# Kernel tuning notes

Hardware: AMD Instinct MI355X
Metric: run time of the kernel (lower is better)

## Reference

```python
import jax, jax.numpy as jnp
import numpy as np

B, N, CIN = 8, 1024, 2048
HID, HC, LV = 1024, 64, 512
NH_SSD, HD, DS = 16, 128, 64
DCONV = 4

def layernorm(x, w, b, eps=1e-5):
    m = x.mean(-1, keepdims=True)
    v = ((x - m) ** 2).mean(-1, keepdims=True)
    return (x - m) * jax.lax.rsqrt(v + eps) * w + b

def rmsnorm(x, w, eps=1e-5):
    return x * jax.lax.rsqrt((x * x).mean(-1, keepdims=True) + eps) * w

def segsum(a):
    # a: (..., T) -> (..., T, T); [i,j] = sum_{j<k<=i} a[k]; -inf above diagonal
    T = a.shape[-1]
    cs = jnp.cumsum(a, -1)
    seg = cs[..., :, None] - cs[..., None, :]
    i = jnp.arange(T)
    return jnp.where(i[:, None] >= i[None, :], seg, -jnp.inf)

def mha(x, Wq, Wk, Wv, Wo, Wo_b, nh=4):
    b, s, h = x.shape
    hd = h // nh
    q = (x @ Wq.T).reshape(b, s, nh, hd).transpose(0, 2, 1, 3)
    k = (x @ Wk.T).reshape(b, s, nh, hd).transpose(0, 2, 1, 3)
    v = (x @ Wv.T).reshape(b, s, nh, hd).transpose(0, 2, 1, 3)
    att = jax.nn.softmax(jnp.einsum('bhqd,bhkd->bhqk', q, k) / jnp.sqrt(jnp.float32(hd)), axis=-1)
    o = jnp.einsum('bhqk,bhkd->bhqd', att, v).transpose(0, 2, 1, 3).reshape(b, s, h)
    return o @ Wo.T + Wo_b

def ssd_minimal(X, A, Bv, Cv, Lc):
    # faithful ssd_minimal_discrete; Bv/Cv have ngroups=1 broadcast to heads (torch einsum broadcasts size-1 labels)
    b, T, h, p = X.shape
    c = T // Lc
    n = Bv.shape[-1]
    X = X.reshape(b, c, Lc, h, p)
    A = A.reshape(b, c, Lc, h).transpose(0, 3, 1, 2)  # b h c l
    Bv = jnp.broadcast_to(Bv.reshape(b, c, Lc, 1, n), (b, c, Lc, h, n))
    Cv = jnp.broadcast_to(Cv.reshape(b, c, Lc, 1, n), (b, c, Lc, h, n))
    cs = jnp.cumsum(A, -1)
    Lmat = jnp.exp(segsum(A))  # b h c l s
    Yd = jnp.einsum('bclhn,bcshn,bhcls,bcshp->bclhp', Cv, Bv, Lmat, X)
    dstates = jnp.exp(cs[..., -1:] - cs)
    st = jnp.einsum('bclhn,bhcl,bclhp->bchpn', Bv, dstates, X)
    st = jnp.concatenate([jnp.zeros_like(st[:, :1]), st], axis=1)
    dchunk = jnp.exp(segsum(jnp.pad(cs[..., -1], ((0, 0), (0, 0), (1, 0)))))
    st = jnp.einsum('bhzc,bchpn->bzhpn', dchunk, st)[:, :-1]
    Yo = jnp.einsum('bclhn,bchpn,bhcl->bclhp', Cv, st, jnp.exp(cs))
    return (Yd + Yo).reshape(b, T, h, p)

def ssd_block(xc, xproj_W, dt_bias, A_log, D):
    b, l, d = xc.shape
    dtBC = xc @ xproj_W.T
    dt = jax.nn.softplus(dtBC[..., :NH_SSD] + dt_bias)
    Bm = dtBC[..., NH_SSD:NH_SSD + DS]
    Cm = dtBC[..., NH_SSD + DS:]
    A = -jnp.exp(A_log)
    X = xc.reshape(b, l, NH_SSD, HD) * dt[..., None]
    Y = ssd_minimal(X, A * dt, Bm, Cm, l)  # single chunk: Lc = seqlen (as in SSD.forward)
    return Y.reshape(b, l, d) + xc * jnp.repeat(D, HD)

@jax.custom_vjp
def round3(y):
    return jnp.round(y)

def _r3_fwd(y):
    return jnp.round(y), y

def _r3_bwd(y, g):
    return (g * (y != 0).astype(g.dtype),)

round3.defvjp(_r3_fwd, _r3_bwd)

def _forward(x, ln0_w, ln0_b, in_W, rms_w, exp_W, conv_W, xproj_W, dt_bias, A_log, D,
             outp_W, outp_b, n1_w, n1_b, aWq, aWk, aWv, aWo, aWo_b,
             h_W, h_b, h_lnw, h_lnb, mask_token, e2d_W, dn_w, dn_b,
             bWq, bWk, bWv, bWo, bWo_b, dout_W, dout_b, mask):
    b = x.shape[0]
    # visible tokens: mask==False; stable argsort keeps original order (== x[~mask].reshape(B,-1,C))
    vis = jnp.argsort(mask.astype(jnp.int32), axis=1)[:, :LV]
    xv = jnp.take_along_axis(x, vis[:, :, None], axis=1)
    xv = layernorm(xv, ln0_w, ln0_b)
    h = xv @ in_W.T
    t = h
    h = rmsnorm(h, rms_w)
    xz = h @ exp_W.T
    xs, z = xz[..., :2 * HID], xz[..., 2 * HID:]
    xc = jax.lax.conv_general_dilated(
        xs.transpose(0, 2, 1), conv_W, (1,), [(DCONV - 1, DCONV - 1)],
        dimension_numbers=('NCH', 'OIH', 'NCH'), feature_group_count=HID)[:, :, :LV].transpose(0, 2, 1)
    y = ssd_block(xc, xproj_W, dt_bias, A_log, D)
    y = y * jax.nn.silu(z)
    y = y @ outp_W.T + outp_b + t
    y = y + mha(layernorm(y, n1_w, n1_b), aWq, aWk, aWv, aWo, aWo_b)
    # hash layer: LN -> hard sigmoid -> straight-through round -> {-1,+1}
    hc = layernorm(y @ h_W.T + h_b, h_lnw, h_lnb)
    hc = 2.0 * round3(jnp.clip((hc + 1.0) / 2.0, 0.0, 1.0)) - 1.0
    # decoder: visible codes + mask tokens
    Lm = N - LV
    dx = jnp.concatenate([hc, jnp.broadcast_to(mask_token, (b, Lm, HC))], axis=1)
    dx = dx @ e2d_W.T
    dx = dx + mha(layernorm(dx, dn_w, dn_b), bWq, bWk, bWv, bWo, bWo_b)
    out = dx @ dout_W.T + dout_b
    return out[:, -Lm:]

def setup_inputs():
    key = jax.random.key(0)
    ks = jax.random.split(key, 20)
    r = lambda i, shape, s=0.02: jax.random.normal(ks[i], shape, dtype=jnp.float32) * s
    x = jax.random.normal(ks[0], (B, N, CIN), dtype=jnp.float32)
    mask = jnp.concatenate([jnp.zeros((B, LV), bool), jnp.ones((B, N - LV), bool)], axis=1)
    A = jax.random.uniform(ks[1], (NH_SSD,), minval=1.0, maxval=16.0)
    return dict(
        x=x,
        ln0_w=jnp.ones(CIN), ln0_b=jnp.zeros(CIN),
        in_W=r(2, (HID, CIN)),
        rms_w=jnp.ones(HID),
        exp_W=r(3, (4 * HID, HID)),
        conv_W=r(4, (2 * HID, 2, DCONV), 0.1),
        xproj_W=r(5, (NH_SSD + 2 * DS, 2 * HID)),
        dt_bias=jnp.zeros(NH_SSD), A_log=jnp.log(A), D=jnp.ones(NH_SSD),
        outp_W=r(6, (HID, 2 * HID)), outp_b=jnp.zeros(HID),
        n1_w=jnp.ones(HID), n1_b=jnp.zeros(HID),
        aWq=r(7, (HID, HID)), aWk=r(8, (HID, HID)), aWv=r(9, (HID, HID)),
        aWo=r(10, (HID, HID)), aWo_b=jnp.zeros(HID),
        h_W=r(11, (HC, HID)), h_b=jnp.zeros(HC),
        h_lnw=jnp.ones(HC), h_lnb=jnp.zeros(HC),
        mask_token=jnp.zeros((1, 1, HC)),
        e2d_W=r(12, (HID, HC)),
        dn_w=jnp.ones(HID), dn_b=jnp.zeros(HID),
        bWq=r(13, (HID, HID)), bWk=r(14, (HID, HID)), bWv=r(15, (HID, HID)),
        bWo=r(16, (HID, HID)), bWo_b=jnp.zeros(HID),
        dout_W=r(17, (CIN, HID)), dout_b=jnp.zeros(CIN),
        mask=mask)

def reference(x, ln0_w, ln0_b, in_W, rms_w, exp_W, conv_W, xproj_W, dt_bias, A_log, D,
              outp_W, outp_b, n1_w, n1_b, aWq, aWk, aWv, aWo, aWo_b,
              h_W, h_b, h_lnw, h_lnb, mask_token, e2d_W, dn_w, dn_b,
              bWq, bWk, bWv, bWo, bWo_b, dout_W, dout_b, mask):
    return _forward(x, ln0_w, ln0_b, in_W, rms_w, exp_W, conv_W, xproj_W, dt_bias, A_log, D,
                    outp_W, outp_b, n1_w, n1_b, aWq, aWk, aWv, aWo, aWo_b,
                    h_W, h_b, h_lnw, h_lnb, mask_token, e2d_W, dn_w, dn_b,
                    bWq, bWk, bWv, bWo, bWo_b, dout_W, dout_b, mask)
```

## Files before the change

kernel.cpp:

```cpp
#include <hip/hip_runtime.h>


typedef short bf16x8 __attribute__((ext_vector_type(8)));
typedef float f32x4 __attribute__((ext_vector_type(4)));

__device__ __forceinline__ unsigned short bf16_rne(float f) {
    unsigned u = __float_as_uint(f);
    unsigned r = u + 0x7FFFu + ((u >> 16) & 1u);
    return (unsigned short)(r >> 16);
}
__device__ __forceinline__ float bf16_tof(unsigned short h) {
    return __uint_as_float(((unsigned)h) << 16);
}
__device__ __forceinline__ void store_pair(unsigned short* dst, long long row,
                                           int width, int c, float v) {
    unsigned short hi = bf16_rne(v);
    unsigned short lo = bf16_rne(v - bf16_tof(hi));
    long long base = row * (2LL * width);
    dst[base + c] = hi;
    dst[base + width + c] = lo;
}
__device__ __forceinline__ void async_ld16(const unsigned short* g, unsigned short* l) {
    __builtin_amdgcn_global_load_lds(
        (const __attribute__((address_space(1))) unsigned int*)g,
        (__attribute__((address_space(3))) unsigned int*)l, 16, 0, 0);
}

__device__ __forceinline__ void xcd_remap(int& bx, int& by) {
    const int Gx = gridDim.x;
    const int nwg = Gx * gridDim.y;
    if ((nwg & 7) != 0) return;
    int lin = bx + Gx * by;
    int logical = (lin & 7) * (nwg >> 3) + (lin >> 3);
    bx = logical % Gx;
    by = logical / Gx;
}

__device__ __forceinline__ float block_sum256(float v) {
    #pragma unroll
    for (int o = 32; o > 0; o >>= 1) v += __shfl_xor(v, o, 64);
    __shared__ float sm[4];
    int w = threadIdx.x >> 6;
    __syncthreads();
    if ((threadIdx.x & 63) == 0) sm[w] = v;
    __syncthreads();
    return sm[0] + sm[1] + sm[2] + sm[3];
}
__device__ __forceinline__ float block_max256(float v) {
    #pragma unroll
    for (int o = 32; o > 0; o >>= 1) v = fmaxf(v, __shfl_xor(v, o, 64));
    __shared__ float smx[4];
    int w = threadIdx.x >> 6;
    __syncthreads();
    if ((threadIdx.x & 63) == 0) smx[w] = v;
    __syncthreads();
    return fmaxf(fmaxf(smx[0], smx[1]), fmaxf(smx[2], smx[3]));
}

template<int NPASS, int OUT, bool DIRECT>
__global__ __launch_bounds__(256, 2) void gemm_bf16_k(
    int M, int N, int K,
    const unsigned short* __restrict__ A2, int lda2, int aLo, long long sAb, long long sAh,
    const unsigned short* __restrict__ B2, int ldb2, int bLo, long long sBb, long long sBh,
    void* __restrict__ Cv, int ldc, int cLo, long long sCb, long long sCh,
    const float* __restrict__ bias, const float* __restrict__ res, int ldr,
    float alpha, int nh)
{
    constexpr int ST   = DIRECT ? 32 : 40;
    constexpr int NARR = (NPASS == 3) ? 4 : 2;
    constexpr int NB   = DIRECT ? 2 : 1;
    constexpr int O_AH = 0;
    constexpr int O_BH = 128 * ST;
    constexpr int O_AL = 2 * 128 * ST;
    constexpr int O_BL = 3 * 128 * ST;
    constexpr int BUFSZ = 128 * ST * NARR;
    __shared__ unsigned short SM[NB * BUFSZ];

    const int z  = blockIdx.z;
    const int bb = z / nh, hh = z - bb * nh;
    A2 += bb * sAb + hh * sAh;
    B2 += bb * sBb + hh * sBh;

    int bx = blockIdx.x, by = blockIdx.y;
    xcd_remap(bx, by);
    const int t    = threadIdx.x;
    const int m0   = by * 128;
    const int n0   = bx * 128;
    const int lane = t & 63, wave = t >> 6;
    const int wm   = (wave >> 1) * 64, wn = (wave & 1) * 64;
    const int lr   = lane & 15, quad = lane >> 4;

    f32x4 acc[4][4];
    #pragma unroll
    for (int i = 0; i < 4; ++i)
        #pragma unroll
        for (int j = 0; j < 4; ++j) acc[i][j] = (f32x4){0.f, 0.f, 0.f, 0.f};

    if constexpr (DIRECT) {
        const int drow  = lane >> 2;
        const int dcswz = (((lane & 3) ^ ((lane >> 2) & 3) ^ ((lane >> 4) & 3)) << 3);
        const int rsw   = ((quad ^ ((lr & 3) ^ (lr >> 2))) << 3);

        auto stage = [&](int k0, int buf) {
            unsigned short* bp = &SM[buf * BUFSZ];
            #pragma unroll
            for (int j = 0; j < 2; ++j) {
                int rr = wave * 32 + j * 16;
                int gr = rr + drow;
                const unsigned short* gA = A2 + (long long)(m0 + gr) * lda2 + k0 + dcswz;
                async_ld16(gA, &bp[O_AH + rr * 32]);
                if (NPASS == 3) async_ld16(gA + aLo, &bp[O_AL + rr * 32]);
                const unsigned short* gB = B2 + (long long)(n0 + gr) * ldb2 + k0 + dcswz;
                async_ld16(gB, &bp[O_BH + rr * 32]);
                if (NPASS == 3) async_ld16(gB + bLo, &bp[O_BL + rr * 32]);
            }
        };

        const int nt = K >> 5;
        stage(0, 0);
        int cur = 0;
        for (int it = 0; it < nt; ++it) {
            asm volatile("s_waitcnt vmcnt(0)" ::: "memory");
            __builtin_amdgcn_s_barrier();
            if (it + 1 < nt) stage((it + 1) << 5, cur ^ 1);

            const unsigned short* bp = &SM[cur * BUFSZ];
            bf16x8 ah[4], bh[4], al[4], bl[4];
            #pragma unroll
            for (int i = 0; i < 4; ++i) {
                int ra = O_AH + (wm + i * 16 + lr) * 32 + rsw;
                int rb = O_BH + (wn + i * 16 + lr) * 32 + rsw;
                ah[i] = *(const bf16x8*)&bp[ra];
                bh[i] = *(const bf16x8*)&bp[rb];
                if (NPASS == 3) {
                    al[i] = *(const bf16x8*)&bp[ra + (O_AL - O_AH)];
                    bl[i] = *(const bf16x8*)&bp[rb + (O_BL - O_BH)];
                }
            }
            #pragma unroll
            for (int mi = 0; mi < 4; ++mi)
                #pragma unroll
                for (int ni = 0; ni < 4; ++ni) {
                    acc[mi][ni] = __builtin_amdgcn_mfma_f32_16x16x32_bf16(
                        ah[mi], bh[ni], acc[mi][ni], 0, 0, 0);
                    if (NPASS == 3) {
                        acc[mi][ni] = __builtin_amdgcn_mfma_f32_16x16x32_bf16(
                            al[mi], bh[ni], acc[mi][ni], 0, 0, 0);
                        acc[mi][ni] = __builtin_amdgcn_mfma_f32_16x16x32_bf16(
                            ah[mi], bl[ni], acc[mi][ni], 0, 0, 0);
                    }
                }
            cur ^= 1;
        }
    } else {
        const int srow = t >> 2;
        const int scol = (t & 3) * 8;

        for (int k0 = 0; k0 < K; k0 += 32) {
            __syncthreads();
            #pragma unroll
            for (int half = 0; half < 2; ++half) {
                int r = srow + half * 64;
                const unsigned short* pA = A2 + (long long)(m0 + r) * lda2 + k0 + scol;
                *(uint4*)&SM[O_AH + r * ST + scol] = *(const uint4*)pA;
                if (NPASS == 3)
                    *(uint4*)&SM[O_AL + r * ST + scol] = *(const uint4*)(pA + aLo);
                int rb = n0 + r;
                uint4 vh = {0u, 0u, 0u, 0u}, vl = {0u, 0u, 0u, 0u};
                if (rb < N) {
                    const unsigned short* pB = B2 + (long long)rb * ldb2 + k0 + scol;
                    vh = *(const uint4*)pB;
                    if (NPASS == 3) vl = *(const uint4*)(pB + bLo);
                }
                *(uint4*)&SM[O_BH + r * ST + scol] = vh;
                if (NPASS == 3) *(uint4*)&SM[O_BL + r * ST + scol] = vl;
            }
            __syncthreads();

            bf16x8 ah[4], bh[4], al[4], bl[4];
            #pragma unroll
            for (int i = 0; i < 4; ++i) {
                int ra = (wm + i * 16 + lr) * ST + quad * 8;
                int rb = (wn + i * 16 + lr) * ST + quad * 8;
                ah[i] = *(const bf16x8*)&SM[O_AH + ra];
                bh[i] = *(const bf16x8*)&SM[O_BH + rb];
                if (NPASS == 3) {
                    al[i] = *(const bf16x8*)&SM[O_AL + ra];
                    bl[i] = *(const bf16x8*)&SM[O_BL + rb];
                }
            }
            #pragma unroll
            for (int mi = 0; mi < 4; ++mi)
                #pragma unroll
                for (int ni = 0; ni < 4; ++ni) {
                    acc[mi][ni] = __builtin_amdgcn_mfma_f32_16x16x32_bf16(
                        ah[mi], bh[ni], acc[mi][ni], 0, 0, 0);
                    if (NPASS == 3) {
                        acc[mi][ni] = __builtin_amdgcn_mfma_f32_16x16x32_bf16(
                            al[mi], bh[ni], acc[mi][ni], 0, 0, 0);
                        acc[mi][ni] = __builtin_amdgcn_mfma_f32_16x16x32_bf16(
                            ah[mi], bl[ni], acc[mi][ni], 0, 0, 0);
                    }
                }
        }
    }

    if (OUT == 0) {
        float* C = (float*)Cv + bb * sCb + hh * sCh;
        #pragma unroll
        for (int mi = 0; mi < 4; ++mi)
            #pragma unroll
            for (int ni = 0; ni < 4; ++ni) {
                int col = n0 + wn + ni * 16 + lr;
                if (col >= N) continue;
                float bv = bias ? bias[col] : 0.f;
                #pragma unroll
                for (int r = 0; r < 4; ++r) {
                    int row = m0 + wm + mi * 16 + quad * 4 + r;
                    float v = alpha * acc[mi][ni][r] + bv;
                    if (res) v += res[(long long)row * ldr + col];
                    C[(long long)row * ldc + col] = v;
                }
            }
    } else if (OUT == 1) {
        unsigned short* C = (unsigned short*)Cv + bb * sCb + hh * sCh;
        #pragma unroll
        for (int mi = 0; mi < 4; ++mi)
            #pragma unroll
            for (int ni = 0; ni < 4; ++ni) {
                int col = n0 + wn + ni * 16 + lr;
                if (col >= N) continue;
                float bv = bias ? bias[col] : 0.f;
                #pragma unroll
                for (int r = 0; r < 4; ++r) {
                    int row = m0 + wm + mi * 16 + quad * 4 + r;
                    float v = alpha * acc[mi][ni][r] + bv;
                    if (res) v += res[(long long)row * ldr + col];
                    unsigned short hi = bf16_rne(v);
                    unsigned short lo = bf16_rne(v - bf16_tof(hi));
                    long long p = (long long)row * ldc + col;
                    C[p] = hi;
                    C[p + cLo] = lo;
                }
            }
    } else {
        unsigned short* C = (unsigned short*)Cv;
        #pragma unroll
        for (int mi = 0; mi < 4; ++mi)
            #pragma unroll
            for (int ni = 0; ni < 4; ++ni) {
                int col = n0 + wn + ni * 16 + lr;
                if (col >= N) continue;
                int row0 = m0 + wm + mi * 16 + quad * 4;
                int b = row0 >> 9, seq0 = row0 & 511;
                ushort4 h4, l4;
// ... 174 lines not shown
            if (rb < N) {
                const unsigned short* pB = B2 + (long long)rb * ldb2 + k0 + scol;
                vh = *(const uint4*)pB;
                if (NPASS == 3) vl = *(const uint4*)(pB + bLo);
            }
            *(uint4*)&Bh[r * ST + scol] = vh;
            if (NPASS == 3) *(uint4*)&Bl[r * ST + scol] = vl;
        }
        __syncthreads();

        bf16x8 ah[4], bh[4], al[4], bl[4];
        #pragma unroll
        for (int i = 0; i < 4; ++i) {
            int ra = (wm + i * 16 + lr) * ST + quad * 8;
            int rb = (wn + i * 16 + lr) * ST + quad * 8;
            ah[i] = *(const bf16x8*)&Ah[ra];
            bh[i] = *(const bf16x8*)&Bh[rb];
            if (NPASS == 3) {
                al[i] = *(const bf16x8*)&Al[ra];
                bl[i] = *(const bf16x8*)&Bl[rb];
            }
        }
        #pragma unroll
        for (int mi = 0; mi < 4; ++mi)
            #pragma unroll
            for (int ni = 0; ni < 4; ++ni) {
                acc[mi][ni] = __builtin_amdgcn_mfma_f32_16x16x32_bf16(
                    ah[mi], bh[ni], acc[mi][ni], 0, 0, 0);
                if (NPASS == 3) {
                    acc[mi][ni] = __builtin_amdgcn_mfma_f32_16x16x32_bf16(
                        al[mi], bh[ni], acc[mi][ni], 0, 0, 0);
                    acc[mi][ni] = __builtin_amdgcn_mfma_f32_16x16x32_bf16(
                        ah[mi], bl[ni], acc[mi][ni], 0, 0, 0);
                }
            }
    }

    float* Cc = C + (long long)blockIdx.z * sCk;
    #pragma unroll
    for (int mi = 0; mi < 4; ++mi)
        #pragma unroll
        for (int ni = 0; ni < 4; ++ni) {
            int col = n0 + wn + ni * 16 + lr;
            if (col >= N) continue;
            #pragma unroll
            for (int r = 0; r < 4; ++r) {
                int row = m0 + wm + mi * 16 + quad * 4 + r;
                Cc[(long long)row * N + col] = acc[mi][ni][r];
            }
        }
}


__global__ __launch_bounds__(256) void skred_rms_k(
    const float* __restrict__ P, long long sCk,
    float* __restrict__ T, unsigned short* __restrict__ HR2,
    const float* __restrict__ w)
{
    long long r = blockIdx.x;
    const int t = threadIdx.x;
    long long base = r * 1024 + t * 4;
    float4 a = *(const float4*)&P[base];
    float4 bq = *(const float4*)&P[sCk + base];
    float v[4] = {a.x + bq.x, a.y + bq.y, a.z + bq.z, a.w + bq.w};
    *(float4*)&T[base] = *(float4*)v;
    float s = v[0]*v[0] + v[1]*v[1] + v[2]*v[2] + v[3]*v[3];
    s = block_sum256(s);
    float rs = 1.f / sqrtf(s * (1.f / 1024.f) + 1e-5f);
    #pragma unroll
    for (int e = 0; e < 4; ++e) {
        int c = t * 4 + e;
        store_pair(HR2, r, 1024, c, v[e] * rs * w[c]);
    }
}

__global__ __launch_bounds__(256) void skred_ln_k(
    const float* __restrict__ P, long long sCk,
    const float* __restrict__ bias, const float* __restrict__ res,
    float* __restrict__ Y1, unsigned short* __restrict__ LNY2,
    const float* __restrict__ w, const float* __restrict__ b)
{
    long long r = blockIdx.x;
    const int t = threadIdx.x;
    long long base = r * 1024 + t * 4;
    float4 a  = *(const float4*)&P[base];
    float4 bq = *(const float4*)&P[sCk + base];
    float4 rv = *(const float4*)&res[base];
    float4 bi = *(const float4*)&bias[t * 4];
    float v[4] = {a.x + bq.x + rv.x + bi.x, a.y + bq.y + rv.y + bi.y,
                  a.z + bq.z + rv.z + bi.z, a.w + bq.w + rv.w + bi.w};
    *(float4*)&Y1[base] = *(float4*)v;
    float s = v[0] + v[1] + v[2] + v[3];
    s = block_sum256(s);
    float m = s * (1.f / 1024.f);
    float vs = 0.f;
    #pragma unroll
    for (int e = 0; e < 4; ++e) { float d = v[e] - m; vs += d * d; }
    vs = block_sum256(vs);
    float rs = 1.f / sqrtf(vs * (1.f / 1024.f) + 1e-5f);
    #pragma unroll
    for (int e = 0; e < 4; ++e) {
        int c = t * 4 + e;
        store_pair(LNY2, r, 1024, c, (v[e] - m) * rs * w[c] + b[c]);
    }
}

__global__ __launch_bounds__(256) void skred_dt_k(
    const float* __restrict__ P, long long sCk,
    const float* __restrict__ dt_bias,
    float* __restrict__ dtBC, float* __restrict__ DT, long long n)
{
    long long idx = (long long)blockIdx.x * 256 + threadIdx.x;
    if (idx >= n) return;
// ... 176 lines not shown
        if (nt > 1) asm volatile("s_waitcnt vmcnt(4)" ::: "memory");
        else        asm volatile("s_waitcnt vmcnt(0)" ::: "memory");
        asm volatile("s_waitcnt lgkmcnt(0)" ::: "memory");
        __builtin_amdgcn_s_barrier();

        for (int it = 0; it < nt; ++it) {
            const int xb = it % 3;
            const int wb = it & 1;
            if (it + 1 < nt) gen_load((it + 1) << 5);
            if (it + 2 < nt) stageX((it + 2) << 5, (it + 2) % 3);

            bf16x8 ah = *(const bf16x8*)&Wh[wb][fbase];
            bf16x8 al = *(const bf16x8*)&Wl[wb][fbase];
            const unsigned short* xhp = &Xh[xb][0];
            const unsigned short* xlp = &Xl[xb][0];
            #pragma unroll
            for (int ni = 0; ni < 8; ++ni) {
                int base = (ni * 16 + lr) * 32 + xsw;
                bf16x8 bh = *(const bf16x8*)&xhp[base];
                bf16x8 bl = *(const bf16x8*)&xlp[base];
                acc[ni] = __builtin_amdgcn_mfma_f32_16x16x32_bf16(
                    ah, bh, acc[ni], 0, 0, 0);
                acc[ni] = __builtin_amdgcn_mfma_f32_16x16x32_bf16(
                    al, bh, acc[ni], 0, 0, 0);
                acc[ni] = __builtin_amdgcn_mfma_f32_16x16x32_bf16(
                    ah, bl, acc[ni], 0, 0, 0);
            }
            if (it + 1 < nt) gen_finish((it + 1) << 5, wb ^ 1);
            if (it + 2 < nt) asm volatile("s_waitcnt vmcnt(4)" ::: "memory");
            else             asm volatile("s_waitcnt vmcnt(0)" ::: "memory");
            asm volatile("s_waitcnt lgkmcnt(0)" ::: "memory");
            __builtin_amdgcn_s_barrier();
        }

        const int row0 = m0 + wave * 16 + quad * 4;
        #pragma unroll
        for (int ni = 0; ni < 8; ++ni) {
            int chan = h * 128 + ni * 16 + lr;
            #pragma unroll
            for (int r = 0; r < 4; ++r) {
                long long row = (long long)(b * 512 + row0 + r);
                float zz = Z[row * 2048 + chan];
                float y = acc[ni][r] * (zz / (1.f + expf(-zz)));
                store_pair(YS2, row, 2048, chan, y);
            }
        }
    }
}

__global__ __launch_bounds__(256) void gemm_f32_k(
    int M, int N, int K,
    const float* __restrict__ A, int lda, long long sAb,
    const float* __restrict__ B, int ldb, long long sBb,
    float* __restrict__ C, int ldc, long long sCb)
{
    __shared__ float As[32][132];
    __shared__ float Bs[32][132];
    const int z = blockIdx.z;
    A += z * sAb; B += z * sBb; C += z * sCb;
    const int n0 = blockIdx.x * 128;
    const int m0 = blockIdx.y * 128;
    const int t  = threadIdx.x;
    const int tx = t & 15, ty = t >> 4;

    float acc[4][16];
    #pragma unroll
    for (int a = 0; a < 4; ++a)
        #pragma unroll
        for (int q = 0; q < 16; ++q) acc[a][q] = 0.f;

    const int ka = (t & 7) << 2;
    const int ra = t >> 3;

    for (int k0 = 0; k0 < K; k0 += 32) {
        __syncthreads();
        #pragma unroll
        for (int i = 0; i < 4; ++i) {
            int row = m0 + ra + i * 32;
            float4 v = *(const float4*)(A + (long long)row * lda + (k0 + ka));
            As[ka + 0][ra + i * 32] = v.x;
            As[ka + 1][ra + i * 32] = v.y;
            As[ka + 2][ra + i * 32] = v.z;
            As[ka + 3][ra + i * 32] = v.w;
            int rowb = n0 + ra + i * 32;
            float4 w = *(const float4*)(B + (long long)rowb * ldb + (k0 + ka));
            Bs[ka + 0][ra + i * 32] = w.x;
            Bs[ka + 1][ra + i * 32] = w.y;
            Bs[ka + 2][ra + i * 32] = w.z;
            Bs[ka + 3][ra + i * 32] = w.w;
        }
        __syncthreads();
        #pragma unroll
        for (int kk = 0; kk < 32; ++kk) {
            float a[8], bm[8];
            *(float4*)&a[0]  = *(const float4*)&As[kk][ty * 4];
            *(float4*)&a[4]  = *(const float4*)&As[kk][64 + ty * 4];
            *(float4*)&bm[0] = *(const float4*)&Bs[kk][tx * 4];
            *(float4*)&bm[4] = *(const float4*)&Bs[kk][64 + tx * 4];
            #pragma unroll
            for (int ri = 0; ri < 2; ++ri)
                #pragma unroll
                for (int ci = 0; ci < 2; ++ci)
                    #pragma unroll
                    for (int i = 0; i < 4; ++i)
                        #pragma unroll
                        for (int j = 0; j < 4; ++j)
                            acc[ri * 2 + ci][i * 4 + j] =
                                fmaf(a[ri * 4 + i], bm[ci * 4 + j], acc[ri * 2 + ci][i * 4 + j]);
        }
    }
    #pragma unroll
    for (int ri = 0; ri < 2; ++ri)
        #pragma unroll
        for (int ci = 0; ci < 2; ++ci) {
            int colb = n0 + ci * 64 + tx * 4;
            #pragma unroll
            for (int i = 0; i < 4; ++i) {
                int row = m0 + ri * 64 + ty * 4 + i;
                *(float4*)(C + (long long)row * ldc + colb) =
                    *(float4*)&acc[ri * 2 + ci][i * 4];
            }
        }
}

__global__ __launch_bounds__(256) void pairify_k(
    const float* __restrict__ src, unsigned short* __restrict__ dst,
    int k_log2, long long n)
{
    long long idx = (long long)blockIdx.x * 256 + threadIdx.x;
    if (idx >= n) return;
    long long r = idx >> k_log2;
    int c = (int)(idx & ((1 << k_log2) - 1));
    store_pair(dst, r, 1 << k_log2, c, src[idx]);
}

struct PairSegs {
    const float* src[7];
    unsigned short* dst[7];
    long long n[7];
    int klog2[7];
};
__global__ __launch_bounds__(256) void pairify_multi_k(PairSegs segs)
{
    int sg = blockIdx.y;
    long long idx = (long long)blockIdx.x * 256 + threadIdx.x;
    if (idx >= segs.n[sg]) return;
    int kl = segs.klog2[sg];
    long long r = idx >> kl;
    int c = (int)(idx & ((1LL << kl) - 1));
    store_pair(segs.dst[sg], r, 1 << kl, c, segs.src[sg][idx]);
}

template<int NE>
__global__ __launch_bounds__(256) void layernorm_pair_v_k(
    const float* __restrict__ in, unsigned short* __restrict__ out2,
    const float* __restrict__ w, const float* __restrict__ b,
    int rows_per_b, long long in_bstride)
{
    const int width = NE * 256;
    long long r = blockIdx.x;
    const float* x = in + (r / rows_per_b) * in_bstride
                   + (r % rows_per_b) * (long long)width;
    const int t = threadIdx.x;
    float v[NE];
    float s = 0.f;
    #pragma unroll
    for (int j = 0; j < NE / 4; ++j) {
        float4 f = *(const float4*)(x + j * 1024 + t * 4);
        v[j * 4 + 0] = f.x; v[j * 4 + 1] = f.y;
        v[j * 4 + 2] = f.z; v[j * 4 + 3] = f.w;
        s += f.x + f.y + f.z + f.w;
    }
    s = block_sum256(s);
    float m = s / (float)width;
    float vs = 0.f;
    #pragma unroll
    for (int e = 0; e < NE; ++e) { float d = v[e] - m; vs += d * d; }
    vs = block_sum256(vs);
    float rs = 1.f / sqrtf(vs / (float)width + 1e-5f);
    #pragma unroll
    for (int j = 0; j < NE / 4; ++j)
        #pragma unroll
        for (int e = 0; e < 4; ++e) {
            int c = j * 1024 + t * 4 + e;
            store_pair(out2, r, width, c, (v[j * 4 + e] - m) * rs * w[c] + b[c]);
        }
}

__global__ __launch_bounds__(256) void softmax_pair_k(float* __restrict__ S,
                                                      unsigned short* __restrict__ P2)
{
    long long r = blockIdx.x;
    float* x = S + r * 512;
    unsigned short* p = P2 + r * 1024;
    int t = threadIdx.x;
    float v0 = x[t], v1 = x[t + 256];
    float mx = block_max256(fmaxf(v0, v1));
    v0 = expf(v0 - mx); v1 = expf(v1 - mx);
    float sum = block_sum256(v0 + v1);
    float inv = 1.f / sum;
    v0 *= inv; v1 *= inv;
    __syncthreads();
    unsigned short h0 = bf16_rne(v0);
    p[t] = h0;       p[512 + t] = bf16_rne(v0 - bf16_tof(h0));
    unsigned short h1 = bf16_rne(v1);
    p[t + 256] = h1; p[512 + t + 256] = bf16_rne(v1 - bf16_tof(h1));
}

__global__ __launch_bounds__(256) void conv_k(
    const float* __restrict__ XS, const float* __restrict__ W,
    unsigned short* __restrict__ XC2, unsigned short* __restrict__ XCT2)
{
    __shared__ float tile[64][65];
    const int o0  = blockIdx.x * 64;
    const int tt0 = blockIdx.y * 64;
    const int b   = blockIdx.z;
    const int t   = threadIdx.x;

    const int o  = o0 + (t & 63);
    const int g2 = (o >> 1) << 1;
    const float* Wo = W + o * 8;
    float w0 = Wo[0], w1 = Wo[1], w2 = Wo[2], w3 = Wo[3];
    float w4 = Wo[4], w5 = Wo[5], w6 = Wo[6], w7 = Wo[7];
    #pragma unroll
    for (int i = 0; i < 16; ++i) {
        int sl = (t >> 6) + 4 * i;
        int tt = tt0 + sl;
        const float* xb = XS + ((long long)(b * 512 + tt)) * 2048 + g2;
        float acc = w3 * xb[0] + w7 * xb[1];
        if (tt >= 1) acc += w2 * xb[-2048] + w6 * xb[-2047];
        if (tt >= 2) acc += w1 * xb[-4096] + w5 * xb[-4095];
        if (tt >= 3) acc += w0 * xb[-6144] + w4 * xb[-6143];
        tile[sl][t & 63] = acc;
    }
    __syncthreads();
    #pragma unroll
    for (int i = 0; i < 16; ++i) {
        int idx = t + 256 * i;
        int sl = idx >> 6, ol = idx & 63;
        float v = tile[sl][ol];
        unsigned short hi = bf16_rne(v);
        unsigned short lo = bf16_rne(v - bf16_tof(hi));
        long long row = (long long)(b * 512 + tt0 + sl);
        XC2[row * 4096 + o0 + ol] = hi;
        XC2[row * 4096 + 2048 + o0 + ol] = lo;
    }
    #pragma unroll
    for (int i = 0; i < 16; ++i) {
        int idx = t + 256 * i;
        int cl = idx >> 6, s = idx & 63;
        float v = tile[s][cl];
        unsigned short hi = bf16_rne(v);
        unsigned short lo = bf16_rne(v - bf16_tof(hi));
        long long tb = (long long)b * 2097152 + (long long)(o0 + cl) * 1024 + tt0 + s;
        XCT2[tb] = hi;
        XCT2[tb + 512] = lo;
    }
}

__global__ __launch_bounds__(64) void cuma_k(
    const float* __restrict__ DT, const float* __restrict__ A_log, float* __restrict__ CUMA)
{
    int h = blockIdx.x, b = blockIdx.y;
    int ln = threadIdx.x;
    float Ah = -expf(A_log[h]);
    float v[8];
    float run = 0.f;
    #pragma unroll
    for (int i = 0; i < 8; ++i) {
        run += Ah * DT[((b * 512) + (ln * 8 + i)) * 16 + h];
        v[i] = run;
    }
    float tot = run;
    float sc = tot;
    #pragma unroll
    for (int o = 1; o <= 32; o <<= 1) {
        float u = __shfl_up(sc, o, 64);
        if (ln >= o) sc += u;
    }
    float excl = sc - tot;
    #pragma unroll
    for (int i = 0; i < 8; ++i)
        CUMA[(b * 16 + h) * 512 + ln * 8 + i] = excl + v[i];
}

__global__ __launch_bounds__(256) void dxm_ln_k(
    const float* __restrict__ mtok, const float* __restrict__ e2d,
    const float* __restrict__ w, const float* __restrict__ b,
    float* __restrict__ dxm, float* __restrict__ lnm)
{
    __shared__ float dx[1024];
    const int t = threadIdx.x;
    float mv[64];
    #pragma unroll
    for (int j = 0; j < 64; ++j) mv[j] = mtok[j];
    float loc[4];
    #pragma unroll
    for (int q = 0; q < 4; ++q) {
        int c = q * 256 + t;
        const float* er = e2d + (long long)c * 64;
        float acc = 0.f;
        #pragma unroll
        for (int j = 0; j < 64; ++j) acc = fmaf(mv[j], er[j], acc);
        loc[q] = acc;
        dx[c] = acc;
        dxm[c] = acc;
    }
    float s = loc[0] + loc[1] + loc[2] + loc[3];
    s = block_sum256(s);
    float m = s * (1.f / 1024.f);
    float vs = 0.f;
    #pragma unroll
    for (int q = 0; q < 4; ++q) { float d = loc[q] - m; vs += d * d; }
    vs = block_sum256(vs);
    float rs = 1.f / sqrtf(vs * (1.f / 1024.f) + 1e-5f);
    #pragma unroll
    for (int q = 0; q < 4; ++q) {
        int c = q * 256 + t;
        lnm[c] = (loc[q] - m) * rs * w[c] + b[c];
    }
}

__global__ __launch_bounds__(256) void projm_k(
    const float* __restrict__ lnm,
    const float* __restrict__ bWq, const float* __restrict__ bWk, const float* __restrict__ bWv,
    float* __restrict__ qm, float* __restrict__ km, float* __restrict__ vm)
{
    int idx = blockIdx.x * 256 + threadIdx.x;
    int sel = idx >> 10, c = idx & 1023;
    const float* W = (sel == 0) ? bWq : (sel == 1) ? bWk : bWv;
    float* O = (sel == 0) ? qm : (sel == 1) ? km : vm;
    const float* wr = W + (long long)c * 1024;
    float acc = 0.f;
    for (int j = 0; j < 1024; j += 4) {
        float4 a = *(const float4*)(lnm + j);
        float4 w4 = *(const float4*)(wr + j);
        acc = fmaf(a.x, w4.x, fmaf(a.y, w4.y, fmaf(a.z, w4.z, fmaf(a.w, w4.w, acc))));
    }
    O[c] = acc;
}

__global__ __launch_bounds__(256) void dec_attn_k(
    const float* __restrict__ KVm,
    const float* __restrict__ qm, const float* __restrict__ km,
    const float* __restrict__ vm, float* __restrict__ OBm)
{
    int h = blockIdx.x, b = blockIdx.y;
    int t = threadIdx.x;
    __shared__ __align__(16) float qs[256];
    __shared__ __align__(16) float ps[512];
    qs[t] = qm[h * 256 + t];
    __syncthreads();
    float s[2];
    #pragma unroll
    for (int i = 0; i < 2; ++i) {
        int r = t + i * 256;
        const float* kr = KVm + ((long long)(b * 512 + r)) * 2048 + h * 256;
        float acc = 0.f;
        for (int c = 0; c < 256; c += 4) {
            float4 k4 = *(const float4*)(kr + c);
            float4 q4 = *(const float4*)(qs + c);
            acc = fmaf(k4.x, q4.x, fmaf(k4.y, q4.y, fmaf(k4.z, q4.z, fmaf(k4.w, q4.w, acc))));
        }
        s[i] = acc * (1.f / 16.f);
    }
    float accm = 0.f;
    for (int c = 0; c < 256; c += 4) {
        float4 k4 = *(const float4*)(km + h * 256 + c);
        float4 q4 = *(const float4*)(qs + c);
        accm = fmaf(k4.x, q4.x, fmaf(k4.y, q4.y, fmaf(k4.z, q4.z, fmaf(k4.w, q4.w, accm))));
    }
    float smv = accm * (1.f / 16.f);
// ... 114 lines not shown
    unsigned short* XCT2    = (unsigned short*)S1;
    float*          POUTP   = S1;
    float*          SA      = S1;
    unsigned short* P2      = (unsigned short*)S1;
    float*          KVm     = S1;
    unsigned short* in_W2   = (unsigned short*)S2;
    float*          XS      = S2;
    unsigned short* YS2     = (unsigned short*)S2;
    float*          PX      = S2;
    unsigned short* QKA2    = (unsigned short*)S2;
    unsigned short* XC2     = (unsigned short*)S3;
    float*          PIN     = S3;
    unsigned short* outp_W2 = (unsigned short*)S3;
    float*          PATT    = S3;
    float*          PH      = S3;
    float*          DXV     = S3;
    unsigned short* LNDXV2  = (unsigned short*)(S3 + 4194304);
    float*          Z       = S4;
    unsigned short* aWq2    = (unsigned short*)S4;
    unsigned short* aWk2    = (unsigned short*)S4 + 2097152;
    unsigned short* aWv2    = (unsigned short*)S4 + 4194304;
    unsigned short* aWo2    = (unsigned short*)S4 + 6291456;
    unsigned short* bWk2    = (unsigned short*)S4 + 8388608;
    unsigned short* bWv2    = (unsigned short*)S4 + 10485760;
    float*          T       = S5;
    unsigned short* Y22     = (unsigned short*)S5;
    unsigned short* HR2     = (unsigned short*)S6;
    float*          Y1      = S6;
    unsigned short* LNY2    = (unsigned short*)S7;
    unsigned short* OA2     = (unsigned short*)S7;
    unsigned short* VT2     = (unsigned short*)S9;

    float* dtBC = SP;
    float* DT   = SP + 589824;
    float* CUMA = SP + 655360;
    float* G    = SP + 720896;
    unsigned short* xprojW2 = (unsigned short*)(SP + 2818048);
    unsigned short* hW2     = (unsigned short*)(SP + 3112960);
    unsigned short* e2dW2   = (unsigned short*)(SP + 3178496);
    unsigned short* HCQ2 = (unsigned short*)(SP + 983040);
    float* dxm  = SP + 1245184;
    float* lnm  = SP + 1246208;
    float* qm   = SP + 1247232;
    float* km   = SP + 1248256;
    float* vm   = SP + 1249280;
    float* OBm  = SP + 1250304;
    float* ydm  = SP + 1258496;
    float* outm = SP + 1266688;

    const long long LL0 = 0;
    const long long P4M = 4194304;
    #define G3D(OUTM, GX, GY, GZ, ...) \
        gemm_bf16_k<3, OUTM, true><<<dim3(GX, GY, GZ), 256, 0, stream>>>(__VA_ARGS__)
    #define G1D(OUTM, GX, GY, GZ, ...) \
        gemm_bf16_k<1, OUTM, true><<<dim3(GX, GY, GZ), 256, 0, stream>>>(__VA_ARGS__)

    {
        PairSegs sA = {};
        sA.src[0] = in_W;    sA.dst[0] = in_W2;   sA.n[0] = 1024LL * 2048; sA.klog2[0] = 11;
        sA.src[1] = xproj_W; sA.dst[1] = xprojW2; sA.n[1] = 144LL * 2048;  sA.klog2[1] = 11;
        sA.src[2] = h_W;     sA.dst[2] = hW2;     sA.n[2] = 64LL * 1024;   sA.klog2[2] = 10;
        sA.src[3] = e2d_W;   sA.dst[3] = e2dW2;   sA.n[3] = 1024LL * 64;   sA.klog2[3] = 6;
        pairify_multi_k<<<dim3(8192, 4), 256, 0, stream>>>(sA);
    }

    layernorm_pair_v_k<8><<<4096, 256, 0, stream>>>(x, XV2, ln0_w, ln0_b, 512,
                                                    (long long)1024 * 2048);
    gemm_bf16_skd_k<3, 0><<<dim3(8, 32, 2), 256, 0, stream>>>(
        1024, 1024, XV2, 4096, 2048, in_W2, 4096, 2048, PIN, P4M);
    skred_rms_k<<<4096, 256, 0, stream>>>(PIN, P4M, T, HR2, rms_w);
    pairify_k<<<16384, 256, 0, stream>>>(exp_W, exp_W2, 10, 4096LL * 1024);
    G3D(0, 16, 32, 2, 4096, 2048, 1024, HR2, 2048, 1024, LL0, LL0,
        exp_W2, 2048, 1024, (long long)2048 * 2048, LL0,
        XS, 2048, 0, 16777216LL, LL0,
        nullptr, nullptr, 0, 1.f, 1);
    conv_k<<<dim3(32, 8, 8), 256, 0, stream>>>(XS, conv_W, XC2, XCT2);
    gemm_bf16_sk_k<3><<<dim3(2, 32, 8), 256, 0, stream>>>(
        144, 256, XC2, 4096, 2048, xprojW2, 4096, 2048, PX, 589824LL);
    skred_dt_k<<<2304, 256, 0, stream>>>(PX, 589824LL, dt_bias, dtBC, DT,
                                         589824LL);
    cuma_k<<<dim3(16, 8), 64, 0, stream>>>(DT, A_log, CUMA);
    gemm_f32_k<<<dim3(4, 4, 8), 256, 0, stream>>>(
        512, 512, 64, dtBC + 80, 144, (long long)512 * 144,
        dtBC + 16, 144, (long long)512 * 144, G, 512, (long long)512 * 512);
    ssd_mfma_k<<<dim3(4, 16, 8), 256, 0, stream>>>(G, CUMA, DT, XCT2, Z, Dv, YS2);

    {
        PairSegs sB = {};
        sB.src[0] = outp_W; sB.dst[0] = outp_W2; sB.n[0] = 1024LL * 2048; sB.klog2[0] = 11;
        sB.src[1] = aWq;    sB.dst[1] = aWq2;    sB.n[1] = 1024LL * 1024; sB.klog2[1] = 10;
        sB.src[2] = aWk;    sB.dst[2] = aWk2;    sB.n[2] = 1024LL * 1024; sB.klog2[2] = 10;
        sB.src[3] = aWv;    sB.dst[3] = aWv2;    sB.n[3] = 1024LL * 1024; sB.klog2[3] = 10;
        sB.src[4] = aWo;    sB.dst[4] = aWo2;    sB.n[4] = 1024LL * 1024; sB.klog2[4] = 10;
        sB.src[5] = bWk;    sB.dst[5] = bWk2;    sB.n[5] = 1024LL * 1024; sB.klog2[5] = 10;
        sB.src[6] = bWv;    sB.dst[6] = bWv2;    sB.n[6] = 1024LL * 1024; sB.klog2[6] = 10;
        pairify_multi_k<<<dim3(8192, 7), 256, 0, stream>>>(sB);
    }

    gemm_bf16_skd_k<3, 0><<<dim3(8, 32, 2), 256, 0, stream>>>(
        1024, 1024, YS2, 4096, 2048, outp_W2, 4096, 2048, POUTP, P4M);
    skred_ln_k<<<4096, 256, 0, stream>>>(POUTP, P4M, outp_b, T, Y1, LNY2,
                                         n1_w, n1_b);

    G3D(1, 16, 32, 1, 4096, 2048, 1024, LNY2, 2048, 1024, LL0, LL0,
        aWq2, 2048, 1024, LL0, LL0, QKA2, 4096, 2048, LL0, LL0,
        nullptr, nullptr, 0, 1.f, 1);
    gemm_bf16_skd_k<3, 1><<<dim3(8, 32, 2), 256, 0, stream>>>(
        1024, 512, LNY2, 2048, 1024, aWv2, 2048, 1024, PATT, P4M);
    skredT_k<<<16384, 256, 0, stream>>>(PATT, P4M, 2, VT2, P4M);
    G3D(0, 4, 4, 32, 512, 512, 256,
        QKA2, 4096, 2048, (long long)512 * 4096, 256,
        QKA2 + 1024, 4096, 2048, (long long)512 * 4096, 256,
        SA, 512, 0, (long long)4 * 512 * 512, (long long)512 * 512,
        nullptr, nullptr, 0, 1.f / 16.f, 4);
    softmax_pair_k<<<16384, 256, 0, stream>>>(SA, P2);
    G3D(1, 2, 4, 32, 512, 256, 512,
        P2, 1024, 512, (long long)4 * 512 * 1024, (long long)512 * 1024,
        VT2, 1024, 512, (long long)1024 * 1024, (long long)256 * 1024,
        OA2, 2048, 1024, (long long)512 * 2048, 256,
        nullptr, nullptr, 0, 1.f, 4);
    gemm_bf16_skd_k<3, 0><<<dim3(8, 32, 2), 256, 0, stream>>>(
        1024, 512, OA2, 2048, 1024, aWo2, 2048, 1024, PATT, P4M);
    skredP_k<<<16384, 256, 0, stream>>>(PATT, P4M, 2, aWo_b, Y1, Y22, P4M);

    gemm_bf16_sk_k<3><<<dim3(1, 32, 8), 256, 0, stream>>>(
        64, 128, Y22, 2048, 1024, hW2, 2048, 1024, PH, 262144LL);
    skred_hc_k<<<4096, 64, 0, stream>>>(PH, 262144LL, h_b, h_lnw, h_lnb, HCQ2);

    G3D(0, 8, 32, 1, 4096, 1024, 64, HCQ2, 128, 64, LL0, LL0,
        e2dW2, 128, 64, LL0, LL0, DXV, 1024, 0, LL0, LL0,
        nullptr, nullptr, 0, 1.f, 1);
    dxm_ln_k<<<1, 256, 0, stream>>>(mtok, e2d_W, dn_w, dn_b, dxm, lnm);
    layernorm_pair_v_k<4><<<4096, 256, 0, stream>>>(DXV, LNDXV2, dn_w, dn_b,
                                                    4096, LL0);
    projm_k<<<12, 256, 0, stream>>>(lnm, bWq, bWk, bWv, qm, km, vm);
    G1D(0, 16, 32, 1, 4096, 2048, 1024, LNDXV2, 2048, 1024, LL0, LL0,
        bWk2, 2048, 1024, LL0, LL0, KVm, 2048, 0, LL0, LL0,
        nullptr, nullptr, 0, 1.f, 1);
    dec_attn_k<<<dim3(4, 8), 256, 0, stream>>>(KVm, qm, km, vm, OBm);
    ydm_k<<<32, 256, 0, stream>>>(OBm, bWo, bWo_b, dxm, ydm);
    outm_k<<<64, 256, 0, stream>>>(ydm, dout_W, dout_b, outm);
    bcast_k<<<8192, 256, 0, stream>>>(outm, out);
    #undef G3D
    #undef G1D
}
```

Before: 1.032 ms.

## Merge small kernels into combined launches and add 2-pass GEMM for e2d

Several independent launches are folded into shared grids. Weight pairification joins the input layernorm in one kernel and the exp_W split joins the RMS reduction in another. The cumsum kernel rides along in extra z-blocks of the f32 Gram GEMM, and the mask-token projection joins the decoder layernorm. A new NPASS=2 GEMM variant drops the lo*hi term for the e2d projection, where the activation side is treated as exact, which cuts one third of its MFMAs. This lowers launch overhead and tail idle time, at the risk of extra precision loss if the A operand's low half is not actually zero.

New measurement: 1.023 ms, median of 2. No clear change (-0.9%).

```diff
diff --git a/kernel.cpp b/kernel.cpp
--- a/kernel.cpp
+++ b/kernel.cpp
@@ -67,12 +67,12 @@
     float alpha, int nh)
 {
     constexpr int ST   = DIRECT ? 32 : 40;
-    constexpr int NARR = (NPASS == 3) ? 4 : 2;
+    constexpr int NARR = (NPASS == 3) ? 4 : ((NPASS == 2) ? 3 : 2);
     constexpr int NB   = DIRECT ? 2 : 1;
     constexpr int O_AH = 0;
     constexpr int O_BH = 128 * ST;
     constexpr int O_AL = 2 * 128 * ST;
-    constexpr int O_BL = 3 * 128 * ST;
+    constexpr int O_BL = ((NPASS == 3) ? 3 : 2) * 128 * ST;
     constexpr int BUFSZ = 128 * ST * NARR;
     __shared__ unsigned short SM[NB * BUFSZ];
 
@@ -112,7 +112,7 @@
                 if (NPASS == 3) async_ld16(gA + aLo, &bp[O_AL + rr * 32]);
                 const unsigned short* gB = B2 + (long long)(n0 + gr) * ldb2 + k0 + dcswz;
                 async_ld16(gB, &bp[O_BH + rr * 32]);
-                if (NPASS == 3) async_ld16(gB + bLo, &bp[O_BL + rr * 32]);
+                if (NPASS >= 2) async_ld16(gB + bLo, &bp[O_BL + rr * 32]);
             }
         };
 
@@ -132,10 +132,8 @@
                 int rb = O_BH + (wn + i * 16 + lr) * 32 + rsw;
                 ah[i] = *(const bf16x8*)&bp[ra];
                 bh[i] = *(const bf16x8*)&bp[rb];
-                if (NPASS == 3) {
-                    al[i] = *(const bf16x8*)&bp[ra + (O_AL - O_AH)];
-                    bl[i] = *(const bf16x8*)&bp[rb + (O_BL - O_BH)];
-                }
+                if (NPASS == 3) al[i] = *(const bf16x8*)&bp[ra + (O_AL - O_AH)];
+                if (NPASS >= 2) bl[i] = *(const bf16x8*)&bp[rb + (O_BL - O_BH)];
             }
             #pragma unroll
             for (int mi = 0; mi < 4; ++mi)
@@ -143,12 +141,12 @@
                 for (int ni = 0; ni < 4; ++ni) {
                     acc[mi][ni] = __builtin_amdgcn_mfma_f32_16x16x32_bf16(
                         ah[mi], bh[ni], acc[mi][ni], 0, 0, 0);
-                    if (NPASS == 3) {
+                    if (NPASS == 3)
                         acc[mi][ni] = __builtin_amdgcn_mfma_f32_16x16x32_bf16(
                             al[mi], bh[ni], acc[mi][ni], 0, 0, 0);
+                    if (NPASS >= 2)
                         acc[mi][ni] = __builtin_amdgcn_mfma_f32_16x16x32_bf16(
                             ah[mi], bl[ni], acc[mi][ni], 0, 0, 0);
-                    }
                 }
             cur ^= 1;
         }
@@ -170,10 +168,10 @@
                 if (rb < N) {
                     const unsigned short* pB = B2 + (long long)rb * ldb2 + k0 + scol;
                     vh = *(const uint4*)pB;
-                    if (NPASS == 3) vl = *(const uint4*)(pB + bLo);
+                    if (NPASS >= 2) vl = *(const uint4*)(pB + bLo);
                 }
                 *(uint4*)&SM[O_BH + r * ST + scol] = vh;
-                if (NPASS == 3) *(uint4*)&SM[O_BL + r * ST + scol] = vl;
+                if (NPASS >= 2) *(uint4*)&SM[O_BL + r * ST + scol] = vl;
             }
             __syncthreads();
 
@@ -184,10 +182,8 @@
                 int rb = (wn + i * 16 + lr) * ST + quad * 8;
                 ah[i] = *(const bf16x8*)&SM[O_AH + ra];
                 bh[i] = *(const bf16x8*)&SM[O_BH + rb];
-                if (NPASS == 3) {
-                    al[i] = *(const bf16x8*)&SM[O_AL + ra];
-                    bl[i] = *(const bf16x8*)&SM[O_BL + rb];
-                }
+                if (NPASS == 3) al[i] = *(const bf16x8*)&SM[O_AL + ra];
+                if (NPASS >= 2) bl[i] = *(const bf16x8*)&SM[O_BL + rb];
             }
             #pragma unroll
             for (int mi = 0; mi < 4; ++mi)
@@ -195,12 +191,12 @@
                 for (int ni = 0; ni < 4; ++ni) {
                     acc[mi][ni] = __builtin_amdgcn_mfma_f32_16x16x32_bf16(
                         ah[mi], bh[ni], acc[mi][ni], 0, 0, 0);
-                    if (NPASS == 3) {
+                    if (NPASS == 3)
                         acc[mi][ni] = __builtin_amdgcn_mfma_f32_16x16x32_bf16(
                             al[mi], bh[ni], acc[mi][ni], 0, 0, 0);
+                    if (NPASS >= 2)
                         acc[mi][ni] = __builtin_amdgcn_mfma_f32_16x16x32_bf16(
                             ah[mi], bl[ni], acc[mi][ni], 0, 0, 0);
-                    }
                 }
         }
     }
@@ -481,13 +477,21 @@
 }
 
 
-__global__ __launch_bounds__(256) void skred_rms_k(
+__global__ __launch_bounds__(256) void skred_rms_pair_k(
     const float* __restrict__ P, long long sCk,
     float* __restrict__ T, unsigned short* __restrict__ HR2,
-    const float* __restrict__ w)
-{
+    const float* __restrict__ w,
+    const float* __restrict__ expW, unsigned short* __restrict__ expW2)
+{
+    const int t = threadIdx.x;
+    if (blockIdx.x >= 4096) {
+        long long idx = (long long)(blockIdx.x - 4096) * 256 + t;
+        long long r = idx >> 10;
+        int c = (int)(idx & 1023);
+        store_pair(expW2, r, 1024, c, expW[idx]);
+        return;
+    }
     long long r = blockIdx.x;
-    const int t = threadIdx.x;
     long long base = r * 1024 + t * 4;
     float4 a = *(const float4*)&P[base];
     float4 bq = *(const float4*)&P[sCk + base];
@@ -770,10 +774,38 @@
     int M, int N, int K,
     const float* __restrict__ A, int lda, long long sAb,
     const float* __restrict__ B, int ldb, long long sBb,
-    float* __restrict__ C, int ldc, long long sCb)
+    float* __restrict__ C, int ldc, long long sCb,
+    const float* __restrict__ DT, const float* __restrict__ A_log,
+    float* __restrict__ CUMA)
 {
     __shared__ float As[32][132];
     __shared__ float Bs[32][132];
+    if (blockIdx.z >= 8) {
+        const int wave = threadIdx.x >> 6;
+        const int ln = threadIdx.x & 63;
+        const int h = blockIdx.y * 4 + blockIdx.x;
+        const int b = (blockIdx.z - 8) * 4 + wave;
+        float Ah = -expf(A_log[h]);
+        float v[8];
+        float run = 0.f;
+        #pragma unroll
+        for (int i = 0; i < 8; ++i) {
+            run += Ah * DT[((b * 512) + (ln * 8 + i)) * 16 + h];
+            v[i] = run;
+        }
+        float tot = run;
+        float sc = tot;
+        #pragma unroll
+        for (int o = 1; o <= 32; o <<= 1) {
+            float u = __shfl_up(sc, o, 64);
+            if (ln >= o) sc += u;
+        }
+        float excl = sc - tot;
+        #pragma unroll
+        for (int i = 0; i < 8; ++i)
+            CUMA[(b * 16 + h) * 512 + ln * 8 + i] = excl + v[i];
+        return;
+    }
     const int z = blockIdx.z;
     A += z * sAb; B += z * sBb; C += z * sCb;
     const int n0 = blockIdx.x * 128;
@@ -841,16 +873,6 @@
         }
 }
 
-__global__ __launch_bounds__(256) void pairify_k(
-    const float* __restrict__ src, unsigned short* __restrict__ dst,
-    int k_log2, long long n)
-{
-    long long idx = (long long)blockIdx.x * 256 + threadIdx.x;
-    if (idx >= n) return;
-    long long r = idx >> k_log2;
-    int c = (int)(idx & ((1 << k_log2) - 1));
-    store_pair(dst, r, 1 << k_log2, c, src[idx]);
-}
 
 struct PairSegs {
     const float* src[7];
@@ -869,40 +891,113 @@
     store_pair(segs.dst[sg], r, 1 << kl, c, segs.src[sg][idx]);
 }
 
-template<int NE>
-__global__ __launch_bounds__(256) void layernorm_pair_v_k(
-    const float* __restrict__ in, unsigned short* __restrict__ out2,
+__global__ __launch_bounds__(256) void prep_a_k(
+    const float* __restrict__ x, unsigned short* __restrict__ XV2,
     const float* __restrict__ w, const float* __restrict__ b,
-    int rows_per_b, long long in_bstride)
-{
-    const int width = NE * 256;
+    PairSegs segs)
+{
+    const int t = threadIdx.x;
+    if (blockIdx.x >= 4096) {
+        int pb = blockIdx.x - 4096;
+        int sg, base;
+        if (pb < 8192)       { sg = 0; base = 0; }
+        else if (pb < 9344)  { sg = 1; base = 8192; }
+        else if (pb < 9600)  { sg = 2; base = 9344; }
+        else                 { sg = 3; base = 9600; }
+        long long idx = (long long)(pb - base) * 256 + t;
+        if (idx >= segs.n[sg]) return;
+        int kl = segs.klog2[sg];
+        long long r = idx >> kl;
+        int c = (int)(idx & ((1LL << kl) - 1));
+        store_pair(segs.dst[sg], r, 1 << kl, c, segs.src[sg][idx]);
+        return;
+    }
     long long r = blockIdx.x;
-    const float* x = in + (r / rows_per_b) * in_bstride
-                   + (r % rows_per_b) * (long long)width;
-    const int t = threadIdx.x;
-    float v[NE];
+    const float* xr = x + (r / 512) * (long long)(1024 * 2048)
+                    + (r % 512) * 2048LL;
+    float v[8];
     float s = 0.f;
     #pragma unroll
-    for (int j = 0; j < NE / 4; ++j) {
-        float4 f = *(const float4*)(x + j * 1024 + t * 4);
+    for (int j = 0; j < 2; ++j) {
+        float4 f = *(const float4*)(xr + j * 1024 + t * 4);
         v[j * 4 + 0] = f.x; v[j * 4 + 1] = f.y;
         v[j * 4 + 2] = f.z; v[j * 4 + 3] = f.w;
         s += f.x + f.y + f.z + f.w;
     }
     s = block_sum256(s);
-    float m = s / (float)width;
+    float m = s * (1.f / 2048.f);
     float vs = 0.f;
     #pragma unroll
-    for (int e = 0; e < NE; ++e) { float d = v[e] - m; vs += d * d; }
+    for (int e = 0; e < 8; ++e) { float d = v[e] - m; vs += d * d; }
     vs = block_sum256(vs);
-    float rs = 1.f / sqrtf(vs / (float)width + 1e-5f);
-    #pragma unroll
-    for (int j = 0; j < NE / 4; ++j)
+    float rs = 1.f / sqrtf(vs * (1.f / 2048.f) + 1e-5f);
+    #pragma unroll
+    for (int j = 0; j < 2; ++j)
         #pragma unroll
         for (int e = 0; e < 4; ++e) {
             int c = j * 1024 + t * 4 + e;
-            store_pair(out2, r, width, c, (v[j * 4 + e] - m) * rs * w[c] + b[c]);
-        }
+            store_pair(XV2, r, 2048, c, (v[j * 4 + e] - m) * rs * w[c] + b[c]);
+        }
+}
+
+__global__ __launch_bounds__(256) void lnd_dxm_k(
+    const float* __restrict__ DXV, unsigned short* __restrict__ LNDXV2,
+    const float* __restrict__ w, const float* __restrict__ b,
+    const float* __restrict__ mtok, const float* __restrict__ e2d,
+    float* __restrict__ dxm, float* __restrict__ lnm)
+{
+    const int t = threadIdx.x;
+    if (blockIdx.x == 4096) {
+        float mv[64];
+        #pragma unroll
+        for (int j = 0; j < 64; ++j) mv[j] = mtok[j];
+        float loc[4];
+        #pragma unroll
+        for (int q = 0; q < 4; ++q) {
+            int c = q * 256 + t;
+            const float* er = e2d + (long long)c * 64;
+            float acc = 0.f;
+            #pragma unroll
+            for (int j = 0; j < 64; ++j) acc = fmaf(mv[j], er[j], acc);
+            loc[q] = acc;
+            dxm[c] = acc;
+        }
+        float s = loc[0] + loc[1] + loc[2] + loc[3];
+        s = block_sum256(s);
+        float m = s * (1.f / 1024.f);
+        float vs = 0.f;
+        #pragma unroll
+        for (int q = 0; q < 4; ++q) { float d = loc[q] - m; vs += d * d; }
+        vs = block_sum256(vs);
+        float rs = 1.f / sqrtf(vs * (1.f / 1024.f) + 1e-5f);
+        #pragma unroll
+        for (int q = 0; q < 4; ++q) {
+            int c = q * 256 + t;
+            lnm[c] = (loc[q] - m) * rs * w[c] + b[c];
+        }
+        return;
+    }
+    long long r = blockIdx.x;
+    const float* xr = DXV + r * 1024LL;
+    float v[4];
+    float s = 0.f;
+    {
+        float4 f = *(const float4*)(xr + t * 4);
+        v[0] = f.x; v[1] = f.y; v[2] = f.z; v[3] = f.w;
+        s = f.x + f.y + f.z + f.w;
+    }
+    s = block_sum256(s);
+    float m = s * (1.f / 1024.f);
+    float vs = 0.f;
+    #pragma unroll
+    for (int e = 0; e < 4; ++e) { float d = v[e] - m; vs += d * d; }
+    vs = block_sum256(vs);
+    float rs = 1.f / sqrtf(vs * (1.f / 1024.f) + 1e-5f);
+    #pragma unroll
+    for (int e = 0; e < 4; ++e) {
+        int c = t * 4 + e;
+        store_pair(LNDXV2, r, 1024, c, (v[e] - m) * rs * w[c] + b[c]);
+    }
 }
 
 __global__ __launch_bounds__(256) void softmax_pair_k(float* __restrict__ S,
@@ -973,69 +1068,6 @@
         long long tb = (long long)b * 2097152 + (long long)(o0 + cl) * 1024 + tt0 + s;
         XCT2[tb] = hi;
         XCT2[tb + 512] = lo;
-    }
-}
-
-__global__ __launch_bounds__(64) void cuma_k(
-    const float* __restrict__ DT, const float* __restrict__ A_log, float* __restrict__ CUMA)
-{
-    int h = blockIdx.x, b = blockIdx.y;
-    int ln = threadIdx.x;
-    float Ah = -expf(A_log[h]);
-    float v[8];
-    float run = 0.f;
-    #pragma unroll
-    for (int i = 0; i < 8; ++i) {
-        run += Ah * DT[((b * 512) + (ln * 8 + i)) * 16 + h];
-        v[i] = run;
-    }
-    float tot = run;
-    float sc = tot;
-    #pragma unroll
-    for (int o = 1; o <= 32; o <<= 1) {
-        float u = __shfl_up(sc, o, 64);
-        if (ln >= o) sc += u;
-    }
-    float excl = sc - tot;
-    #pragma unroll
-    for (int i = 0; i < 8; ++i)
-        CUMA[(b * 16 + h) * 512 + ln * 8 + i] = excl + v[i];
-}
-
-__global__ __launch_bounds__(256) void dxm_ln_k(
-    const float* __restrict__ mtok, const float* __restrict__ e2d,
-    const float* __restrict__ w, const float* __restrict__ b,
-    float* __restrict__ dxm, float* __restrict__ lnm)
-{
-    __shared__ float dx[1024];
-    const int t = threadIdx.x;
-    float mv[64];
-    #pragma unroll
-    for (int j = 0; j < 64; ++j) mv[j] = mtok[j];
-    float loc[4];
-    #pragma unroll
-    for (int q = 0; q < 4; ++q) {
-        int c = q * 256 + t;
-        const float* er = e2d + (long long)c * 64;
-        float acc = 0.f;
-        #pragma unroll
-        for (int j = 0; j < 64; ++j) acc = fmaf(mv[j], er[j], acc);
-        loc[q] = acc;
-        dx[c] = acc;
-        dxm[c] = acc;
-    }
-    float s = loc[0] + loc[1] + loc[2] + loc[3];
-    s = block_sum256(s);
-    float m = s * (1.f / 1024.f);
-    float vs = 0.f;
-    #pragma unroll
-    for (int q = 0; q < 4; ++q) { float d = loc[q] - m; vs += d * d; }
-    vs = block_sum256(vs);
-    float rs = 1.f / sqrtf(vs * (1.f / 1024.f) + 1e-5f);
-    #pragma unroll
-    for (int q = 0; q < 4; ++q) {
-        int c = q * 256 + t;
-        lnm[c] = (loc[q] - m) * rs * w[c] + b[c];
     }
 }
 
@@ -1256,6 +1288,8 @@
     const long long P4M = 4194304;
     #define G3D(OUTM, GX, GY, GZ, ...) \
         gemm_bf16_k<3, OUTM, true><<<dim3(GX, GY, GZ), 256, 0, stream>>>(__VA_ARGS__)
+    #define G2D(OUTM, GX, GY, GZ, ...) \
+        gemm_bf16_k<2, OUTM, true><<<dim3(GX, GY, GZ), 256, 0, stream>>>(__VA_ARGS__)
     #define G1D(OUTM, GX, GY, GZ, ...) \
         gemm_bf16_k<1, OUTM, true><<<dim3(GX, GY, GZ), 256, 0, stream>>>(__VA_ARGS__)
 
@@ -1265,15 +1299,13 @@
         sA.src[1] = xproj_W; sA.dst[1] = xprojW2; sA.n[1] = 144LL * 2048;  sA.klog2[1] = 11;
         sA.src[2] = h_W;     sA.dst[2] = hW2;     sA.n[2] = 64LL * 1024;   sA.klog2[2] = 10;
         sA.src[3] = e2d_W;   sA.dst[3] = e2dW2;   sA.n[3] = 1024LL * 64;   sA.klog2[3] = 6;
-        pairify_multi_k<<<dim3(8192, 4), 256, 0, stream>>>(sA);
-    }
-
-    layernorm_pair_v_k<8><<<4096, 256, 0, stream>>>(x, XV2, ln0_w, ln0_b, 512,
-                                                    (long long)1024 * 2048);
+        prep_a_k<<<4096 + 9856, 256, 0, stream>>>(x, XV2, ln0_w, ln0_b, sA);
+    }
+
     gemm_bf16_skd_k<3, 0><<<dim3(8, 32, 2), 256, 0, stream>>>(
         1024, 1024, XV2, 4096, 2048, in_W2, 4096, 2048, PIN, P4M);
-    skred_rms_k<<<4096, 256, 0, stream>>>(PIN, P4M, T, HR2, rms_w);
-    pairify_k<<<16384, 256, 0, stream>>>(exp_W, exp_W2, 10, 4096LL * 1024);
+    skred_rms_pair_k<<<4096 + 16384, 256, 0, stream>>>(
+        PIN, P4M, T, HR2, rms_w, exp_W, exp_W2);
     G3D(0, 16, 32, 2, 4096, 2048, 1024, HR2, 2048, 1024, LL0, LL0,
         exp_W2, 2048, 1024, (long long)2048 * 2048, LL0,
         XS, 2048, 0, 16777216LL, LL0,
@@ -1283,10 +1315,10 @@
         144, 256, XC2, 4096, 2048, xprojW2, 4096, 2048, PX, 589824LL);
     skred_dt_k<<<2304, 256, 0, stream>>>(PX, 589824LL, dt_bias, dtBC, DT,
                                          589824LL);
-    cuma_k<<<dim3(16, 8), 64, 0, stream>>>(DT, A_log, CUMA);
-    gemm_f32_k<<<dim3(4, 4, 8), 256, 0, stream>>>(
+    gemm_f32_k<<<dim3(4, 4, 10), 256, 0, stream>>>(
         512, 512, 64, dtBC + 80, 144, (long long)512 * 144,
-        dtBC + 16, 144, (long long)512 * 144, G, 512, (long long)512 * 512);
+        dtBC + 16, 144, (long long)512 * 144, G, 512, (long long)512 * 512,
+        DT, A_log, CUMA);
     ssd_mfma_k<<<dim3(4, 16, 8), 256, 0, stream>>>(G, CUMA, DT, XCT2, Z, Dv, YS2);
 
     {
@@ -1331,12 +1363,11 @@
         64, 128, Y22, 2048, 1024, hW2, 2048, 1024, PH, 262144LL);
     skred_hc_k<<<4096, 64, 0, stream>>>(PH, 262144LL, h_b, h_lnw, h_lnb, HCQ2);
 
-    G3D(0, 8, 32, 1, 4096, 1024, 64, HCQ2, 128, 64, LL0, LL0,
+    G2D(0, 8, 32, 1, 4096, 1024, 64, HCQ2, 128, 64, LL0, LL0,
         e2dW2, 128, 64, LL0, LL0, DXV, 1024, 0, LL0, LL0,
         nullptr, nullptr, 0, 1.f, 1);
-    dxm_ln_k<<<1, 256, 0, stream>>>(mtok, e2d_W, dn_w, dn_b, dxm, lnm);
-    layernorm_pair_v_k<4><<<4096, 256, 0, stream>>>(DXV, LNDXV2, dn_w, dn_b,
-                                                    4096, LL0);
+    lnd_dxm_k<<<4097, 256, 0, stream>>>(DXV, LNDXV2, dn_w, dn_b,
+                                        mtok, e2d_W, dxm, lnm);
     projm_k<<<12, 256, 0, stream>>>(lnm, bWq, bWk, bWv, qm, km, vm);
     G1D(0, 16, 32, 1, 4096, 2048, 1024, LNDXV2, 2048, 1024, LL0, LL0,
         bWk2, 2048, 1024, LL0, LL0, KVm, 2048, 0, LL0, LL0,
@@ -1346,5 +1377,6 @@
     outm_k<<<64, 256, 0, stream>>>(ydm, dout_W, dout_b, outm);
     bcast_k<<<8192, 256, 0, stream>>>(outm, out);
     #undef G3D
+    #undef G2D
     #undef G1D
 }
```
